# Kernel tuning notes

Hardware: AMD Instinct MI355X
Metric: run time of the kernel (lower is better)

## Reference

```python
import jax, jax.numpy as jnp
import numpy as np

B, T, L, M = 64, 2000, 400, 80
SIGMA_FACTOR = 0.05
SIGMA_CAP = 10.0
SIGMA_MIN = 1.5
WARMUP_STEPS = 10000
GLOBAL_STEP = 0  # fresh loss module -> progress = 0
ENTROPY_TARGET = 3.5
ATTN_W_START = 1.0
ATTN_W_MIN = 0.2
EPS = 1e-8


def setup_inputs() -> dict:
    key = jax.random.key(0)
    ks = jax.random.split(key, 8)
    mel_out_postnet = jax.random.normal(ks[0], (B, T, M), jnp.float32)
    mel_out = jax.random.normal(ks[1], (B, T, M), jnp.float32)
    gate_out = jax.random.normal(ks[2], (B, T), jnp.float32)
    # alignments: stacked per-step attention, row-normalized like real softmax outputs
    a = jax.random.uniform(ks[3], (B, T, L), jnp.float32)
    alignments = a / jnp.sum(a, axis=-1, keepdims=True)
    mel_target = jax.random.normal(ks[4], (B, T, M), jnp.float32)
    gate_target = jnp.round(jax.random.uniform(ks[5], (B, T), jnp.float32))
    mel_lengths = jax.random.randint(ks[6], (B,), T // 2, T + 1, jnp.int32).at[0].set(T)
    text_lengths = jax.random.randint(ks[7], (B,), L // 2, L + 1, jnp.int32).at[0].set(L)
    return {
        "mel_out_postnet": mel_out_postnet, "mel_out": mel_out, "gate_out": gate_out,
        "alignments": alignments, "mel_target": mel_target, "gate_target": gate_target,
        "mel_lengths": mel_lengths, "text_lengths": text_lengths,
    }


def _diagonal_target(text_lengths):
    # sigma per batch element; global_step=0 -> progress=0 -> sigma = init_sigma
    init_sigma = jnp.clip(text_lengths.astype(jnp.float32) * SIGMA_FACTOR, 3.0, SIGMA_CAP)
    progress = min(1.0, GLOBAL_STEP / float(WARMUP_STEPS))
    sigma = init_sigma - (init_sigma - SIGMA_MIN) * progress  # [B]
    t = jnp.arange(T, dtype=jnp.int32)  # decoder steps
    Lb = text_lengths[:, None]  # [B,1]
    # expected_pos = min(int(t*Lb/T), Lb-1); positive ints -> integer floor div matches trunc
    exp_pos = jnp.minimum((t[None, :] * Lb) // T, Lb - 1).astype(jnp.float32)  # [B,T]
    pos = jnp.arange(L, dtype=jnp.float32)  # [L]
    z = (pos[None, None, :] - exp_pos[:, :, None]) / sigma[:, None, None]
    g = jnp.exp(-0.5 * z * z)  # [B,T,L]
    valid = (pos[None, None, :] < text_lengths[:, None, None].astype(jnp.float32))
    g = g * valid
    return g / (jnp.sum(g, axis=-1, keepdims=True) + EPS)


def reference(mel_out_postnet, mel_out, gate_out, alignments, mel_target,
              gate_target, mel_lengths, text_lengths):
    # masked L1 on mel (mel_target already [B,T,M], matching the torch transpose)
    valid = (jnp.arange(T)[None, :] < mel_lengths[:, None])[:, :, None]  # [B,T,1]
    vf = valid.astype(jnp.float32)
    n_valid = jnp.sum(vf) * M
    mel_loss_1 = jnp.sum(jnp.abs(mel_out - mel_target) * vf) / n_valid
    mel_loss_2 = jnp.sum(jnp.abs(mel_out_postnet - mel_target) * vf) / n_valid
    loss_mel = mel_loss_1 + mel_loss_2

    # BCEWithLogits, mean reduction (stable form)
    x, z_t = gate_out, gate_target
    loss_gate = jnp.mean(jnp.maximum(x, 0.0) - x * z_t + jnp.log1p(jnp.exp(-jnp.abs(x))))

    # guided-attention KL against diagonal Gaussian target
    target = _diagonal_target(text_lengths)  # [B,T,L]
    attn_safe = jnp.maximum(alignments, EPS)
    log_pred = jnp.log(attn_safe)
    kl_pw = jnp.where(target > 0.0, target * (jnp.log(jnp.maximum(target, EPS)) - log_pred), 0.0)
    attention_kl = jnp.sum(kl_pw) / B / T  # batchmean then / T_dec
    attention_kl = jnp.minimum(attention_kl, 150.0)

    # entropy-gated attention weight (python-float in torch -> stop_gradient)
    attn_entropy = jnp.mean(-jnp.sum(attn_safe * log_pred, axis=2))
    ratio = jnp.maximum(attn_entropy / ENTROPY_TARGET, 0.0)
    weight = jnp.where(attn_entropy <= ENTROPY_TARGET,
                       jnp.maximum(ATTN_W_MIN, ATTN_W_START * ratio),
                       ATTN_W_START)
    weight = jax.lax.stop_gradient(weight)

    total_loss = loss_mel + loss_gate + weight * attention_kl
    return (total_loss, loss_mel, loss_gate, attention_kl)
```

## Files before the change

kernel.cpp:

```cpp
#include <hip/hip_runtime.h>
#include <cstddef>
#include <cstdint>

#define B_ 64
#define T_ 2000
#define L_ 400
#define M_ 80
#define EPSF 1e-8f
#define LOG_EPSF -18.420680743952367f

#define NBLK 2048

__device__ inline float waveReduce(float v) {
#pragma unroll
  for (int m = 32; m >= 1; m >>= 1) v += __shfl_xor(v, m, 64);
  return v;
}

__global__ __launch_bounds__(256) void fused_kernel(
    const float4* __restrict__ mo, const float4* __restrict__ mp,
    const float4* __restrict__ mt, const float* __restrict__ gx,
    const float* __restrict__ gz, const float* __restrict__ align,
    const int* __restrict__ mel_lengths, const int* __restrict__ text_lengths,
    double* __restrict__ ws) {
  const int tid = blockIdx.x * 256 + threadIdx.x;
  const int nthreads = NBLK * 256;

  float mel_acc = 0.f;
  const int N4 = B_ * T_ * (M_ / 4);
  for (int i = tid; i < N4; i += nthreads) {
    int row = i / (M_ / 4);
    int b = row / T_;
    int t = row - b * T_;
    if (t < mel_lengths[b]) {
      float4 a = mo[i], c = mp[i], d = mt[i];
      mel_acc += fabsf(a.x - d.x) + fabsf(a.y - d.y) + fabsf(a.z - d.z) + fabsf(a.w - d.w)
               + fabsf(c.x - d.x) + fabsf(c.y - d.y) + fabsf(c.z - d.z) + fabsf(c.w - d.w);
    }
  }

  float gate_acc = 0.f;
  for (int i = tid; i < B_ * T_; i += nthreads) {
    float xv = gx[i], z = gz[i];
    gate_acc += fmaxf(xv, 0.f) - xv * z + log1pf(__expf(-fabsf(xv)));
  }

  const int lane = threadIdx.x & 63;
  const int wib = threadIdx.x >> 6;
  const int waveId = blockIdx.x * 4 + wib;
  const int numWaves = NBLK * 4;
  float kl_acc = 0.f, ent_acc = 0.f;
  for (int p = waveId; p < B_ * T_; p += numWaves) {
    int b = p / T_;
    int t = p - b * T_;
    int Lb = text_lengths[b];
    float sigma = fminf(fmaxf((float)Lb * 0.05f, 3.0f), 10.0f);
    float invsig = 1.0f / sigma;
    int epi = t * Lb / T_;
    int lim = Lb - 1;
    if (epi > lim) epi = lim;
    float ep = (float)epi;
    const float* row = align + (size_t)p * L_;
    float g[7], lp[7], ee[7];
    float S = 0.f;
#pragma unroll
    for (int k = 0; k < 7; ++k) {
      int l = lane + 64 * k;
      g[k] = 0.f; lp[k] = 0.f; ee[k] = 0.f;
      if (l < L_) {
        float a = row[l];
        float as = fmaxf(a, EPSF);
        float lpv = __logf(as);
        lp[k] = lpv;
        ent_acc -= as * lpv;
        float z = ((float)l - ep) * invsig;
        float e = -0.5f * z * z;
        ee[k] = e;
        float gv = (l < Lb) ? __expf(e) : 0.f;
        g[k] = gv;
        S += gv;
      }
    }
    S = waveReduce(S);
    float Se = S + EPSF;
    float inv = 1.0f / Se;
    float logSe = __logf(Se);
#pragma unroll
    for (int k = 0; k < 7; ++k) {
      int l = lane + 64 * k;
      if (l < L_ && g[k] > 0.f) {
        float tgt = g[k] * inv;
        float lt = fmaxf(ee[k] - logSe, LOG_EPSF);
        kl_acc += tgt * (lt - lp[k]);
      }
    }
  }

  float w0 = waveReduce(mel_acc);
  float w1 = waveReduce(gate_acc);
  float w2 = waveReduce(kl_acc);
  float w3 = waveReduce(ent_acc);
  __shared__ double sh[4][4];
  if (lane == 0) {
    sh[wib][0] = (double)w0; sh[wib][1] = (double)w1;
    sh[wib][2] = (double)w2; sh[wib][3] = (double)w3;
  }
  __syncthreads();
  if (threadIdx.x == 0) {
    ws[blockIdx.x]            = sh[0][0] + sh[1][0] + sh[2][0] + sh[3][0];
    ws[NBLK + blockIdx.x]     = sh[0][1] + sh[1][1] + sh[2][1] + sh[3][1];
    ws[2 * NBLK + blockIdx.x] = sh[0][2] + sh[1][2] + sh[2][2] + sh[3][2];
    ws[3 * NBLK + blockIdx.x] = sh[0][3] + sh[1][3] + sh[2][3] + sh[3][3];
  }
}

__device__ double segSum(const double* __restrict__ p, int n, double* sh) {
  double a = 0.0;
  for (int i = threadIdx.x; i < n; i += 256) a += p[i];
  sh[threadIdx.x] = a;
  __syncthreads();
  for (int s = 128; s > 0; s >>= 1) {
    if ((int)threadIdx.x < s) sh[threadIdx.x] += sh[threadIdx.x + s];
    __syncthreads();
  }
  double r = sh[0];
  __syncthreads();
  return r;
}

__global__ __launch_bounds__(256) void finalize_kernel(
    const double* __restrict__ ws, const int* __restrict__ mel_lengths,
    float* __restrict__ out) {
  __shared__ double sh[256];
  double mel_sum  = segSum(ws, NBLK, sh);
  double gate_sum = segSum(ws + NBLK, NBLK, sh);
  double kl_sum   = segSum(ws + 2 * NBLK, NBLK, sh);
  double ent_sum  = segSum(ws + 3 * NBLK, NBLK, sh);
  if (threadIdx.x == 0) {
    long nv = 0;
    for (int b = 0; b < B_; ++b) nv += mel_lengths[b];
    double n_valid = (double)nv * (double)M_;
    float loss_mel  = (float)(mel_sum / n_valid);
    float loss_gate = (float)(gate_sum / (double)(B_ * T_));
    float kl  = (float)(kl_sum / (double)(B_ * T_));
    kl = fminf(kl, 150.0f);
    float ent = (float)(ent_sum / (double)(B_ * T_));
    float ratio = fmaxf(ent / 3.5f, 0.0f);
    float weight = (ent <= 3.5f) ? fmaxf(0.2f, 1.0f * ratio) : 1.0f;
    out[0] = loss_mel + loss_gate + weight * kl;
    out[1] = loss_mel;
    out[2] = loss_gate;
    out[3] = kl;
  }
}

extern "C" void kernel_launch(void* const* d_in, const int* in_sizes, int n_in,
                              void* d_out, int out_size, void* d_ws, size_t ws_size,
                              hipStream_t stream) {
  const float* mel_out_postnet = (const float*)d_in[0];
  const float* mel_out         = (const float*)d_in[1];
  const float* gate_out        = (const float*)d_in[2];
  const float* alignments      = (const float*)d_in[3];
  const float* mel_target      = (const float*)d_in[4];
  const float* gate_target     = (const float*)d_in[5];
  const int*   mel_lengths     = (const int*)d_in[6];
  const int*   text_lengths    = (const int*)d_in[7];
  float* out = (float*)d_out;
  double* ws = (double*)d_ws;

  fused_kernel<<<dim3(NBLK), dim3(256), 0, stream>>>(
      (const float4*)mel_out, (const float4*)mel_out_postnet,
      (const float4*)mel_target, gate_out, gate_target,
      alignments, mel_lengths, text_lengths, ws);
  finalize_kernel<<<dim3(1), dim3(256), 0, stream>>>(ws, mel_lengths, out);
}
```

Before: 389.9 us.

## Precompute per-position Gaussian normalizers in a table and flatten KL loop to float4

Adds a small pre-kernel that computes, for each (batch, expected position) pair, the Gaussian row normalizer (inverse sum, log sum), inverse sigma and position. The fused kernel can then drop the per-row wave reduction and process alignments as a flat float4 grid-stride stream with a table lookup per element. The gate loop is also vectorized to float4. This removes per-row cross-lane reductions and the reliance on one wave per 400-wide row. In exchange it adds an extra kernel launch and a per-element integer division plus a gather from the table.

New measurement: 398.6 us. +2.3%, slower.

```diff
diff --git a/kernel.cpp b/kernel.cpp
--- a/kernel.cpp
+++ b/kernel.cpp
@@ -10,6 +10,7 @@
 #define LOG_EPSF -18.420680743952367f
 
 #define NBLK 2048
+#define TBL_N (B_ * L_)
 
 __device__ inline float waveReduce(float v) {
 #pragma unroll
@@ -17,12 +18,45 @@
   return v;
 }
 
+__global__ __launch_bounds__(256) void table_kernel(
+    const int* __restrict__ text_lengths, float4* __restrict__ tbl) {
+  const int lane = threadIdx.x & 63;
+  const int wid = (blockIdx.x * 256 + threadIdx.x) >> 6;
+  if (wid >= TBL_N) return;
+  const int b = wid / L_;
+  const int epi = wid - b * L_;
+  const int Lb = text_lengths[b];
+  const float sigma = fminf(fmaxf((float)Lb * 0.05f, 3.0f), 10.0f);
+  const float invsig = 1.0f / sigma;
+  const float epf = (float)epi;
+  float S = 0.f;
+#pragma unroll
+  for (int k = 0; k < 7; ++k) {
+    int l = lane + 64 * k;
+    if (l < Lb) {
+      float z = ((float)l - epf) * invsig;
+      S += __expf(-0.5f * z * z);
+    }
+  }
+  S = waveReduce(S);
+  if (lane == 0) {
+    float Se = S + EPSF;
+    float4 e;
+    e.x = 1.0f / Se;
+    e.y = __logf(Se);
+    e.z = invsig;
+    e.w = epf;
+    tbl[wid] = e;
+  }
+}
+
 __global__ __launch_bounds__(256) void fused_kernel(
     const float4* __restrict__ mo, const float4* __restrict__ mp,
-    const float4* __restrict__ mt, const float* __restrict__ gx,
-    const float* __restrict__ gz, const float* __restrict__ align,
+    const float4* __restrict__ mt, const float4* __restrict__ gx,
+    const float4* __restrict__ gz, const float4* __restrict__ align4,
+    const float4* __restrict__ tbl,
     const int* __restrict__ mel_lengths, const int* __restrict__ text_lengths,
-    double* __restrict__ ws) {
+    double* __restrict__ partials) {
   const int tid = blockIdx.x * 256 + threadIdx.x;
   const int nthreads = NBLK * 256;
 
@@ -40,58 +74,41 @@
   }
 
   float gate_acc = 0.f;
-  for (int i = tid; i < B_ * T_; i += nthreads) {
-    float xv = gx[i], z = gz[i];
-    gate_acc += fmaxf(xv, 0.f) - xv * z + log1pf(__expf(-fabsf(xv)));
+  for (int i = tid; i < (B_ * T_) / 4; i += nthreads) {
+    float4 xv = gx[i], zv = gz[i];
+    gate_acc += fmaxf(xv.x, 0.f) - xv.x * zv.x + log1pf(__expf(-fabsf(xv.x)))
+              + fmaxf(xv.y, 0.f) - xv.y * zv.y + log1pf(__expf(-fabsf(xv.y)))
+              + fmaxf(xv.z, 0.f) - xv.z * zv.z + log1pf(__expf(-fabsf(xv.z)))
+              + fmaxf(xv.w, 0.f) - xv.w * zv.w + log1pf(__expf(-fabsf(xv.w)));
   }
 
-  const int lane = threadIdx.x & 63;
-  const int wib = threadIdx.x >> 6;
-  const int waveId = blockIdx.x * 4 + wib;
-  const int numWaves = NBLK * 4;
   float kl_acc = 0.f, ent_acc = 0.f;
-  for (int p = waveId; p < B_ * T_; p += numWaves) {
-    int b = p / T_;
-    int t = p - b * T_;
+  const int NA4 = B_ * T_ * (L_ / 4);
+  for (int i = tid; i < NA4; i += nthreads) {
+    int row = i / (L_ / 4);
+    int li4 = i - row * (L_ / 4);
+    int l0 = li4 * 4;
+    int b = row / T_;
+    int t = row - b * T_;
     int Lb = text_lengths[b];
-    float sigma = fminf(fmaxf((float)Lb * 0.05f, 3.0f), 10.0f);
-    float invsig = 1.0f / sigma;
     int epi = t * Lb / T_;
     int lim = Lb - 1;
     if (epi > lim) epi = lim;
-    float ep = (float)epi;
-    const float* row = align + (size_t)p * L_;
-    float g[7], lp[7], ee[7];
-    float S = 0.f;
+    float4 tb = tbl[b * L_ + epi];
+    float4 a4 = align4[i];
+    float av[4] = {a4.x, a4.y, a4.z, a4.w};
 #pragma unroll
-    for (int k = 0; k < 7; ++k) {
-      int l = lane + 64 * k;
-      g[k] = 0.f; lp[k] = 0.f; ee[k] = 0.f;
-      if (l < L_) {
-        float a = row[l];
-        float as = fmaxf(a, EPSF);
-        float lpv = __logf(as);
-        lp[k] = lpv;
-        ent_acc -= as * lpv;
-        float z = ((float)l - ep) * invsig;
+    for (int j = 0; j < 4; ++j) {
+      float as = fmaxf(av[j], EPSF);
+      float lp = __logf(as);
+      ent_acc -= as * lp;
+      int l = l0 + j;
+      if (l < Lb) {
+        float z = ((float)l - tb.w) * tb.z;
         float e = -0.5f * z * z;
-        ee[k] = e;
-        float gv = (l < Lb) ? __expf(e) : 0.f;
-        g[k] = gv;
-        S += gv;
-      }
-    }
-    S = waveReduce(S);
-    float Se = S + EPSF;
-    float inv = 1.0f / Se;
-    float logSe = __logf(Se);
-#pragma unroll
-    for (int k = 0; k < 7; ++k) {
-      int l = lane + 64 * k;
-      if (l < L_ && g[k] > 0.f) {
-        float tgt = g[k] * inv;
-        float lt = fmaxf(ee[k] - logSe, LOG_EPSF);
-        kl_acc += tgt * (lt - lp[k]);
+        float tgt = __expf(e) * tb.x;
+        float lt = fmaxf(e - tb.y, LOG_EPSF);
+        kl_acc += tgt * (lt - lp);
       }
     }
   }
@@ -101,16 +118,17 @@
   float w2 = waveReduce(kl_acc);
   float w3 = waveReduce(ent_acc);
   __shared__ double sh[4][4];
+  const int lane = threadIdx.x & 63, wib = threadIdx.x >> 6;
   if (lane == 0) {
     sh[wib][0] = (double)w0; sh[wib][1] = (double)w1;
     sh[wib][2] = (double)w2; sh[wib][3] = (double)w3;
   }
   __syncthreads();
   if (threadIdx.x == 0) {
-    ws[blockIdx.x]            = sh[0][0] + sh[1][0] + sh[2][0] + sh[3][0];
-    ws[NBLK + blockIdx.x]     = sh[0][1] + sh[1][1] + sh[2][1] + sh[3][1];
-    ws[2 * NBLK + blockIdx.x] = sh[0][2] + sh[1][2] + sh[2][2] + sh[3][2];
-    ws[3 * NBLK + blockIdx.x] = sh[0][3] + sh[1][3] + sh[2][3] + sh[3][3];
+    partials[blockIdx.x]            = sh[0][0] + sh[1][0] + sh[2][0] + sh[3][0];
+    partials[NBLK + blockIdx.x]     = sh[0][1] + sh[1][1] + sh[2][1] + sh[3][1];
+    partials[2 * NBLK + blockIdx.x] = sh[0][2] + sh[1][2] + sh[2][2] + sh[3][2];
+    partials[3 * NBLK + blockIdx.x] = sh[0][3] + sh[1][3] + sh[2][3] + sh[3][3];
   }
 }
 
@@ -129,13 +147,13 @@
 }
 
 __global__ __launch_bounds__(256) void finalize_kernel(
-    const double* __restrict__ ws, const int* __restrict__ mel_lengths,
+    const double* __restrict__ partials, const int* __restrict__ mel_lengths,
     float* __restrict__ out) {
   __shared__ double sh[256];
-  double mel_sum  = segSum(ws, NBLK, sh);
-  double gate_sum = segSum(ws + NBLK, NBLK, sh);
-  double kl_sum   = segSum(ws + 2 * NBLK, NBLK, sh);
-  double ent_sum  = segSum(ws + 3 * NBLK, NBLK, sh);
+  double mel_sum  = segSum(partials, NBLK, sh);
+  double gate_sum = segSum(partials + NBLK, NBLK, sh);
+  double kl_sum   = segSum(partials + 2 * NBLK, NBLK, sh);
+  double ent_sum  = segSum(partials + 3 * NBLK, NBLK, sh);
   if (threadIdx.x == 0) {
     long nv = 0;
     for (int b = 0; b < B_; ++b) nv += mel_lengths[b];
@@ -166,11 +184,16 @@
   const int*   mel_lengths     = (const int*)d_in[6];
   const int*   text_lengths    = (const int*)d_in[7];
   float* out = (float*)d_out;
-  double* ws = (double*)d_ws;
 
+  float4* tbl = (float4*)d_ws;
+  double* partials = (double*)((char*)d_ws + TBL_N * sizeof(float4));
+
+  table_kernel<<<dim3((TBL_N * 64 + 255) / 256), dim3(256), 0, stream>>>(
+      text_lengths, tbl);
   fused_kernel<<<dim3(NBLK), dim3(256), 0, stream>>>(
       (const float4*)mel_out, (const float4*)mel_out_postnet,
-      (const float4*)mel_target, gate_out, gate_target,
-      alignments, mel_lengths, text_lengths, ws);
-  finalize_kernel<<<dim3(1), dim3(256), 0, stream>>>(ws, mel_lengths, out);
+      (const float4*)mel_target, (const float4*)gate_out,
+      (const float4*)gate_target, (const float4*)alignments, tbl,
+      mel_lengths, text_lengths, partials);
+  finalize_kernel<<<dim3(1), dim3(256), 0, stream>>>(partials, mel_lengths, out);
 }
```
